# Optimization experiments

Hardware: AMD Instinct MI355X
Metric: run time of the kernel (lower is better)

Reference implementation:

```python
import jax, jax.numpy as jnp
import numpy as np

T = 16777216  # series length (2**24)


def setup_inputs() -> dict:
    key = jax.random.key(0)
    k1, k2 = jax.random.split(key)
    timeseries = jax.random.normal(k1, (T,), dtype=jnp.float32)
    # learned smoothing parameter alpha in (0, 1), per min_max_norm(0, 1) constraint
    alpha = jax.random.uniform(k2, (1,), dtype=jnp.float32)
    return {"timeseries": timeseries, "alpha": alpha}


def reference(timeseries, alpha):
    """Simple exponential smoothing (component form).

    level_0 = y_0; level_t = (1-alpha)*level_{t-1} + alpha*y_t for t >= 1.
    prediction_t (the forecast emitted at step t) is the level BEFORE the
    update, so the output is levels[0 : T-1], length T-1 (matches the
    original loop that emits one forecast per timestep in timeseries[1:]).

    Expressed as a first-order linear recurrence s_t = a_t * s_{t-1} + b_t
    and solved with an associative (parallel) scan.
    """
    a0 = alpha[0]
    n = timeseries.shape[0]
    dt = timeseries.dtype
    # a_0 = 0, b_0 = y_0 pins level_0 = y_0 regardless of the dummy carry.
    a = jnp.concatenate([jnp.zeros((1,), dt),
                         jnp.full((n - 1,), 1.0, dt) * (1.0 - a0)])
    b = jnp.concatenate([timeseries[:1], a0 * timeseries[1:]])

    def combine(e1, e2):
        a1, b1 = e1
        a2, b2 = e2
        return (a1 * a2, a2 * b1 + b2)

    _, levels = jax.lax.associative_scan(combine, (a, b))  # levels[t] = level_t
    return levels[:-1]
```

## Files before the change

### kernel.cpp

```cpp
#include <hip/hip_runtime.h>
#include <stdint.h>


#define BLOCK 256
#define SEG   64
#define VPT   (SEG / 4)
#define CHUNK (BLOCK * SEG)
#define ROWS  65

__device__ __forceinline__ void block_scan_affine(float* sa, float* sb, int t) {
#pragma unroll
    for (int off = 1; off < BLOCK; off <<= 1) {
        float pa = 1.0f, pb = 0.0f;
        if (t >= off) { pa = sa[t - off]; pb = sb[t - off]; }
        __syncthreads();
        if (t >= off) {
            float ca = sa[t], cb = sb[t];
            sa[t] = pa * ca;
            sb[t] = fmaf(ca, pb, cb);
        }
        __syncthreads();
    }
}

__global__ __launch_bounds__(BLOCK) void k_block_agg(
    const float* __restrict__ y, const float* __restrict__ alpha_p,
    float* __restrict__ aggA, float* __restrict__ aggB, long n)
{
    const int t = threadIdx.x;
    const long base = (long)blockIdx.x * CHUNK + (long)t * SEG;
    const float alpha = alpha_p[0];
    const float oma = 1.0f - alpha;

    float a = 1.0f, s = 0.0f;
    if (base + SEG <= n) {
        const float4* p = (const float4*)(y + base);
#pragma unroll
        for (int v = 0; v < VPT; ++v) {
            float4 q = p[v];
            s = fmaf(oma, s, alpha * q.x);
            s = fmaf(oma, s, alpha * q.y);
            s = fmaf(oma, s, alpha * q.z);
            s = fmaf(oma, s, alpha * q.w);
            a *= oma; a *= oma; a *= oma; a *= oma;
        }
    } else {
        for (int k = 0; k < SEG; ++k) {
            long idx = base + k;
            if (idx < n) { s = fmaf(oma, s, alpha * y[idx]); a *= oma; }
        }
    }

    __shared__ float sa[BLOCK], sb[BLOCK];
    sa[t] = a; sb[t] = s;
    __syncthreads();
    block_scan_affine(sa, sb, t);
    if (t == BLOCK - 1) {
        aggA[blockIdx.x] = sa[t];
        aggB[blockIdx.x] = sb[t];
    }
}

__global__ __launch_bounds__(BLOCK) void k_carry_scan(
    const float* __restrict__ aggA, const float* __restrict__ aggB,
    const float* __restrict__ y, float* __restrict__ carry, int G)
{
    const int t = threadIdx.x;
    const int items = (G + BLOCK - 1) / BLOCK;
    const float y0 = y[0];

    float ta = 1.0f, tb = 0.0f;
    for (int j = 0; j < items; ++j) {
        int g = t * items + j;
        if (g < G) {
            float ca = aggA[g], cb = aggB[g];
            float na = ta * ca;
            float nb = fmaf(ca, tb, cb);
            ta = na; tb = nb;
        }
    }

    __shared__ float sa[BLOCK], sb[BLOCK];
    sa[t] = ta; sb[t] = tb;
    __syncthreads();
    block_scan_affine(sa, sb, t);

    float ea = 1.0f, eb = 0.0f;
    if (t > 0) { ea = sa[t - 1]; eb = sb[t - 1]; }
    for (int j = 0; j < items; ++j) {
        int g = t * items + j;
        if (g < G) {
            carry[g] = fmaf(ea, y0, eb);
            float ca = aggA[g], cb = aggB[g];
            float na = ea * ca;
            float nb = fmaf(ca, eb, cb);
            ea = na; eb = nb;
        }
    }
}

__global__ __launch_bounds__(BLOCK, 4) void k_emit(
    const float* __restrict__ y, const float* __restrict__ alpha_p,
    const float* __restrict__ carry, float* __restrict__ out, long n)
{
    __shared__ float sa[BLOCK], sb[BLOCK];
    __shared__ float stage[2 * 64 * ROWS];

    const int t = threadIdx.x;
    const long tbase = (long)blockIdx.x * CHUNK;
    const long base  = tbase + (long)t * SEG;
    const float alpha = alpha_p[0];
    const float oma   = 1.0f - alpha;
    const float c     = carry[blockIdx.x];
    const bool fullTile = (tbase + CHUNK <= n);

    float4 arr[VPT];
    float a_seg, b_seg;

    if (fullTile) {
        const float4* p = (const float4*)(y + base);
#pragma unroll
        for (int v = 0; v < VPT; ++v) arr[v] = p[v];
        float s = 0.0f;
#pragma unroll
        for (int v = 0; v < VPT; ++v) {
            s = fmaf(oma, s, alpha * arr[v].x);
            s = fmaf(oma, s, alpha * arr[v].y);
            s = fmaf(oma, s, alpha * arr[v].z);
            s = fmaf(oma, s, alpha * arr[v].w);
        }
        b_seg = s;
        a_seg = __powf(oma, (float)SEG);
    } else {
        float a = 1.0f, s = 0.0f;
        for (int k = 0; k < SEG; ++k) {
            long idx = base + k;
            if (idx < n) { s = fmaf(oma, s, alpha * y[idx]); a *= oma; }
        }
        a_seg = a; b_seg = s;
    }

    sa[t] = a_seg; sb[t] = b_seg;
    __syncthreads();
    block_scan_affine(sa, sb, t);

    float ea = 1.0f, eb = 0.0f;
    if (t > 0) { ea = sa[t - 1]; eb = sb[t - 1]; }
    float lvl = fmaf(ea, c, eb);

    if (fullTile) {
#pragma unroll
        for (int v = 0; v < VPT; ++v) {
            float4 q = arr[v], r;
            lvl = fmaf(oma, lvl, alpha * q.x); r.x = lvl;
            lvl = fmaf(oma, lvl, alpha * q.y); r.y = lvl;
            lvl = fmaf(oma, lvl, alpha * q.z); r.z = lvl;
            lvl = fmaf(oma, lvl, alpha * q.w); r.w = lvl;
            arr[v] = r;
        }
        const int  wv = t >> 6;
        const int  ln = t & 63;
        const bool lastGuard = (tbase + CHUNK > n - 1);
#pragma unroll
        for (int p = 0; p < 2; ++p) {
            __syncthreads();
            if ((wv >> 1) == p) {
                int g = ((wv & 1) << 6) | ln;
                float* row = &stage[g * ROWS];
#pragma unroll
                for (int v = 0; v < VPT; ++v) {
                    row[4 * v + 0] = arr[v].x;
                    row[4 * v + 1] = arr[v].y;
                    row[4 * v + 2] = arr[v].z;
                    row[4 * v + 3] = arr[v].w;
                }
            }
            __syncthreads();
            const long rbase = tbase + (long)p * 8192;
#pragma unroll
            for (int k = 0; k < 8; ++k) {
                int jj = t + (k << 8);
                int g  = jj >> 4;
                int e  = (jj << 2) & 63;
                const float* row = &stage[g * ROWS + e];
                float4 r;
                r.x = row[0]; r.y = row[1]; r.z = row[2]; r.w = row[3];
                long gi = rbase + 4 * (long)jj;
                if (!lastGuard) {
                    *(float4*)(out + gi) = r;
                } else {
                    if (gi + 4 <= n - 1) {
                        *(float4*)(out + gi) = r;
                    } else {
                        if (gi + 0 < n - 1) out[gi + 0] = r.x;
                        if (gi + 1 < n - 1) out[gi + 1] = r.y;
                        if (gi + 2 < n - 1) out[gi + 2] = r.z;
                        if (gi + 3 < n - 1) out[gi + 3] = r.w;
                    }
                }
            }
        }
    } else {
        for (int k = 0; k < SEG; ++k) {
            long idx = base + k;
            if (idx < n) {
                lvl = fmaf(oma, lvl, alpha * y[idx]);
                if (idx < n - 1) out[idx] = lvl;
            }
        }
    }
}

extern "C" void kernel_launch(void* const* d_in, const int* in_sizes, int n_in,
                              void* d_out, int out_size, void* d_ws, size_t ws_size,
                              hipStream_t stream) {
    const float* y     = (const float*)d_in[0];
    const float* alpha = (const float*)d_in[1];
    float* out = (float*)d_out;
    const long n = (long)in_sizes[0];
    const int  G = (int)((n + CHUNK - 1) / CHUNK);

    float* aggA  = (float*)d_ws;
    float* aggB  = aggA + G;
    float* carry = aggB + G;

    k_block_agg<<<G, BLOCK, 0, stream>>>(y, alpha, aggA, aggB, n);
    k_carry_scan<<<1, BLOCK, 0, stream>>>(aggA, aggB, y, carry, G);
    k_emit<<<G, BLOCK, 0, stream>>>(y, alpha, carry, out, n);
}
```

Before: 130.2 us.

## Fuse carry scan into emit kernel, recompute block prefix redundantly per tile

Drops the single-block carry-scan kernel. Each emit block now re-reads all tile aggregates, runs its own block scan over them, and derives its own carry, which removes one launch and the serialized one-block phase between the two big kernels. The cost is redundant reads and scans of the G=1024 aggregates in every block, plus extra syncs. The aggregate kernel also computes the decay product with powf instead of repeated multiplies.

Result: no change. 129.2 us (-0.7%).

```diff
diff --git a/kernel.cpp b/kernel.cpp
--- a/kernel.cpp
+++ b/kernel.cpp
@@ -42,8 +42,8 @@
             s = fmaf(oma, s, alpha * q.y);
             s = fmaf(oma, s, alpha * q.z);
             s = fmaf(oma, s, alpha * q.w);
-            a *= oma; a *= oma; a *= oma; a *= oma;
-        }
+        }
+        a = __powf(oma, (float)SEG);
     } else {
         for (int k = 0; k < SEG; ++k) {
             long idx = base + k;
@@ -61,62 +61,26 @@
     }
 }
 
-__global__ __launch_bounds__(BLOCK) void k_carry_scan(
+__global__ __launch_bounds__(BLOCK, 4) void k_emit_fused(
+    const float* __restrict__ y, const float* __restrict__ alpha_p,
     const float* __restrict__ aggA, const float* __restrict__ aggB,
-    const float* __restrict__ y, float* __restrict__ carry, int G)
-{
-    const int t = threadIdx.x;
-    const int items = (G + BLOCK - 1) / BLOCK;
-    const float y0 = y[0];
-
-    float ta = 1.0f, tb = 0.0f;
-    for (int j = 0; j < items; ++j) {
-        int g = t * items + j;
-        if (g < G) {
-            float ca = aggA[g], cb = aggB[g];
-            float na = ta * ca;
-            float nb = fmaf(ca, tb, cb);
-            ta = na; tb = nb;
-        }
-    }
-
-    __shared__ float sa[BLOCK], sb[BLOCK];
-    sa[t] = ta; sb[t] = tb;
-    __syncthreads();
-    block_scan_affine(sa, sb, t);
-
-    float ea = 1.0f, eb = 0.0f;
-    if (t > 0) { ea = sa[t - 1]; eb = sb[t - 1]; }
-    for (int j = 0; j < items; ++j) {
-        int g = t * items + j;
-        if (g < G) {
-            carry[g] = fmaf(ea, y0, eb);
-            float ca = aggA[g], cb = aggB[g];
-            float na = ea * ca;
-            float nb = fmaf(ca, eb, cb);
-            ea = na; eb = nb;
-        }
-    }
-}
-
-__global__ __launch_bounds__(BLOCK, 4) void k_emit(
-    const float* __restrict__ y, const float* __restrict__ alpha_p,
-    const float* __restrict__ carry, float* __restrict__ out, long n)
+    float* __restrict__ out, long n, int G)
 {
     __shared__ float sa[BLOCK], sb[BLOCK];
     __shared__ float stage[2 * 64 * ROWS];
+    __shared__ float s_carry;
 
     const int t = threadIdx.x;
-    const long tbase = (long)blockIdx.x * CHUNK;
-    const long base  = tbase + (long)t * SEG;
+    const int tile = blockIdx.x;
     const float alpha = alpha_p[0];
     const float oma   = 1.0f - alpha;
-    const float c     = carry[blockIdx.x];
+    const long tbase = (long)tile * CHUNK;
+    const long base  = tbase + (long)t * SEG;
     const bool fullTile = (tbase + CHUNK <= n);
+    const float y0 = y[0];
 
     float4 arr[VPT];
     float a_seg, b_seg;
-
     if (fullTile) {
         const float4* p = (const float4*)(y + base);
 #pragma unroll
@@ -144,18 +108,51 @@
     __syncthreads();
     block_scan_affine(sa, sb, t);
 
-    float ea = 1.0f, eb = 0.0f;
-    if (t > 0) { ea = sa[t - 1]; eb = sb[t - 1]; }
-    float lvl = fmaf(ea, c, eb);
+    float ea_th = 1.0f, eb_th = 0.0f;
+    if (t > 0) { ea_th = sa[t - 1]; eb_th = sb[t - 1]; }
+
+    const int items = (G + BLOCK - 1) / BLOCK;
+    {
+        float ta = 1.0f, tb = 0.0f;
+        for (int j = 0; j < items; ++j) {
+            int g = t * items + j;
+            if (g < G) {
+                float ca = aggA[g], cb = aggB[g];
+                tb = fmaf(ca, tb, cb);
+                ta *= ca;
+            }
+        }
+        __syncthreads();
+        sa[t] = ta; sb[t] = tb;
+        __syncthreads();
+        block_scan_affine(sa, sb, t);
+
+        const int q = tile / items;
+        if (t == q) {
+            float ea = (q > 0) ? sa[q - 1] : 1.0f;
+            float eb = (q > 0) ? sb[q - 1] : 0.0f;
+            const int r = tile - q * items;
+            for (int j = 0; j < r; ++j) {
+                int g = q * items + j;
+                float ca = aggA[g], cb = aggB[g];
+                eb = fmaf(ca, eb, cb);
+                ea *= ca;
+            }
+            s_carry = fmaf(ea, y0, eb);
+        }
+        __syncthreads();
+    }
+
+    float lvl = fmaf(ea_th, s_carry, eb_th);
 
     if (fullTile) {
 #pragma unroll
         for (int v = 0; v < VPT; ++v) {
-            float4 q = arr[v], r;
-            lvl = fmaf(oma, lvl, alpha * q.x); r.x = lvl;
-            lvl = fmaf(oma, lvl, alpha * q.y); r.y = lvl;
-            lvl = fmaf(oma, lvl, alpha * q.z); r.z = lvl;
-            lvl = fmaf(oma, lvl, alpha * q.w); r.w = lvl;
+            float4 q4 = arr[v], r;
+            lvl = fmaf(oma, lvl, alpha * q4.x); r.x = lvl;
+            lvl = fmaf(oma, lvl, alpha * q4.y); r.y = lvl;
+            lvl = fmaf(oma, lvl, alpha * q4.z); r.z = lvl;
+            lvl = fmaf(oma, lvl, alpha * q4.w); r.w = lvl;
             arr[v] = r;
         }
         const int  wv = t >> 6;
@@ -220,11 +217,9 @@
     const long n = (long)in_sizes[0];
     const int  G = (int)((n + CHUNK - 1) / CHUNK);
 
-    float* aggA  = (float*)d_ws;
-    float* aggB  = aggA + G;
-    float* carry = aggB + G;
+    float* aggA = (float*)d_ws;
+    float* aggB = aggA + G;
 
     k_block_agg<<<G, BLOCK, 0, stream>>>(y, alpha, aggA, aggB, n);
-    k_carry_scan<<<1, BLOCK, 0, stream>>>(aggA, aggB, y, carry, G);
-    k_emit<<<G, BLOCK, 0, stream>>>(y, alpha, carry, out, n);
-}
+    k_emit_fused<<<G, BLOCK, 0, stream>>>(y, alpha, aggA, aggB, out, n, G);
+}
```

## Shrink per-thread segment to 16 and restructure staging for higher occupancy

Applied to the files above, without the earlier changes.

Reduces the per-thread segment from 64 to 16 elements, so each block covers 4096 elements and four times as many blocks launch. The emit kernel's LDS staging becomes a single pass with a new row mapping, and both big kernels request 8 blocks per CU. The block aggregate now uses __powf instead of repeated multiplies. The aim is more parallelism and lower register/LDS pressure, at the cost of a larger carry array and more per-element block-scan overhead, including a longer serial loop in the single-block carry scan.

New measurement: 133.9 us. +2.9%, slower.

```diff
diff --git a/kernel.cpp b/kernel.cpp
--- a/kernel.cpp
+++ b/kernel.cpp
@@ -3,7 +3,7 @@
 
 
 #define BLOCK 256
-#define SEG   64
+#define SEG   16
 #define VPT   (SEG / 4)
 #define CHUNK (BLOCK * SEG)
 #define ROWS  65
@@ -23,7 +23,7 @@
     }
 }
 
-__global__ __launch_bounds__(BLOCK) void k_block_agg(
+__global__ __launch_bounds__(BLOCK, 8) void k_block_agg(
     const float* __restrict__ y, const float* __restrict__ alpha_p,
     float* __restrict__ aggA, float* __restrict__ aggB, long n)
 {
@@ -42,8 +42,8 @@
             s = fmaf(oma, s, alpha * q.y);
             s = fmaf(oma, s, alpha * q.z);
             s = fmaf(oma, s, alpha * q.w);
-            a *= oma; a *= oma; a *= oma; a *= oma;
-        }
+        }
+        a = __powf(oma, (float)SEG);
     } else {
         for (int k = 0; k < SEG; ++k) {
             long idx = base + k;
@@ -74,9 +74,8 @@
         int g = t * items + j;
         if (g < G) {
             float ca = aggA[g], cb = aggB[g];
-            float na = ta * ca;
-            float nb = fmaf(ca, tb, cb);
-            ta = na; tb = nb;
+            tb = fmaf(ca, tb, cb);
+            ta *= ca;
         }
     }
 
@@ -92,19 +91,18 @@
         if (g < G) {
             carry[g] = fmaf(ea, y0, eb);
             float ca = aggA[g], cb = aggB[g];
-            float na = ea * ca;
-            float nb = fmaf(ca, eb, cb);
-            ea = na; eb = nb;
-        }
-    }
-}
-
-__global__ __launch_bounds__(BLOCK, 4) void k_emit(
+            eb = fmaf(ca, eb, cb);
+            ea *= ca;
+        }
+    }
+}
+
+__global__ __launch_bounds__(BLOCK, 8) void k_emit(
     const float* __restrict__ y, const float* __restrict__ alpha_p,
     const float* __restrict__ carry, float* __restrict__ out, long n)
 {
     __shared__ float sa[BLOCK], sb[BLOCK];
-    __shared__ float stage[2 * 64 * ROWS];
+    __shared__ float stage[64 * ROWS];
 
     const int t = threadIdx.x;
     const long tbase = (long)blockIdx.x * CHUNK;
@@ -151,52 +149,44 @@
     if (fullTile) {
 #pragma unroll
         for (int v = 0; v < VPT; ++v) {
-            float4 q = arr[v], r;
-            lvl = fmaf(oma, lvl, alpha * q.x); r.x = lvl;
-            lvl = fmaf(oma, lvl, alpha * q.y); r.y = lvl;
-            lvl = fmaf(oma, lvl, alpha * q.z); r.z = lvl;
-            lvl = fmaf(oma, lvl, alpha * q.w); r.w = lvl;
+            float4 q4 = arr[v], r;
+            lvl = fmaf(oma, lvl, alpha * q4.x); r.x = lvl;
+            lvl = fmaf(oma, lvl, alpha * q4.y); r.y = lvl;
+            lvl = fmaf(oma, lvl, alpha * q4.z); r.z = lvl;
+            lvl = fmaf(oma, lvl, alpha * q4.w); r.w = lvl;
             arr[v] = r;
         }
-        const int  wv = t >> 6;
-        const int  ln = t & 63;
+        {
+            float* row = &stage[(t >> 2) * ROWS + ((t & 3) << 4)];
+#pragma unroll
+            for (int v = 0; v < VPT; ++v) {
+                row[4 * v + 0] = arr[v].x;
+                row[4 * v + 1] = arr[v].y;
+                row[4 * v + 2] = arr[v].z;
+                row[4 * v + 3] = arr[v].w;
+            }
+        }
+        __syncthreads();
         const bool lastGuard = (tbase + CHUNK > n - 1);
 #pragma unroll
-        for (int p = 0; p < 2; ++p) {
-            __syncthreads();
-            if ((wv >> 1) == p) {
-                int g = ((wv & 1) << 6) | ln;
-                float* row = &stage[g * ROWS];
-#pragma unroll
-                for (int v = 0; v < VPT; ++v) {
-                    row[4 * v + 0] = arr[v].x;
-                    row[4 * v + 1] = arr[v].y;
-                    row[4 * v + 2] = arr[v].z;
-                    row[4 * v + 3] = arr[v].w;
-                }
-            }
-            __syncthreads();
-            const long rbase = tbase + (long)p * 8192;
-#pragma unroll
-            for (int k = 0; k < 8; ++k) {
-                int jj = t + (k << 8);
-                int g  = jj >> 4;
-                int e  = (jj << 2) & 63;
-                const float* row = &stage[g * ROWS + e];
-                float4 r;
-                r.x = row[0]; r.y = row[1]; r.z = row[2]; r.w = row[3];
-                long gi = rbase + 4 * (long)jj;
-                if (!lastGuard) {
+        for (int k = 0; k < 4; ++k) {
+            int jj = t + (k << 8);
+            int g  = jj >> 4;
+            int e  = (jj << 2) & 63;
+            const float* row = &stage[g * ROWS + e];
+            float4 r;
+            r.x = row[0]; r.y = row[1]; r.z = row[2]; r.w = row[3];
+            long gi = tbase + 4 * (long)jj;
+            if (!lastGuard) {
+                *(float4*)(out + gi) = r;
+            } else {
+                if (gi + 4 <= n - 1) {
                     *(float4*)(out + gi) = r;
                 } else {
-                    if (gi + 4 <= n - 1) {
-                        *(float4*)(out + gi) = r;
-                    } else {
-                        if (gi + 0 < n - 1) out[gi + 0] = r.x;
-                        if (gi + 1 < n - 1) out[gi + 1] = r.y;
-                        if (gi + 2 < n - 1) out[gi + 2] = r.z;
-                        if (gi + 3 < n - 1) out[gi + 3] = r.w;
-                    }
+                    if (gi + 0 < n - 1) out[gi + 0] = r.x;
+                    if (gi + 1 < n - 1) out[gi + 1] = r.y;
+                    if (gi + 2 < n - 1) out[gi + 2] = r.z;
+                    if (gi + 3 < n - 1) out[gi + 3] = r.w;
                 }
             }
         }
```
